# Optimization experiments

Measured on AMD Instinct MI355X. Metric: run time of the kernel, lower is better.

Reference implementation:

```python
import jax, jax.numpy as jnp
import numpy as np

DT = 0.01          # integration timestep
TH_HI = 1.0        # upper firing threshold
TH_LO = -1.0       # lower firing threshold


def setup_inputs() -> dict:
    key = jax.random.key(0)
    inputs = jax.random.normal(key, (64, 256, 1024), dtype=jnp.float32)
    return {"inputs": inputs}


def reference(inputs):
    # inputs: [B, T, D] pre-activation drive at each timestep
    rates = jnp.tanh(inputs)                     # activation(inputs), [B, T, D]
    x = jnp.swapaxes(rates, 0, 1)                # [T, B, D] for scan over time

    def step(v, r):
        v = v + r * DT                           # integrate
        sp = (v >= TH_HI).astype(v.dtype)        # positive spike
        sn = (v <= TH_LO).astype(v.dtype)        # negative spike
        v = v - sp * TH_HI - sn * TH_LO          # subtractive (self-regulating) reset
        out = (sp - sn) / DT                     # signed spike train scaled by 1/dt
        return v, out

    v0 = jnp.zeros(x.shape[1:], dtype=x.dtype)   # initial membrane state
    _, spikes = jax.lax.scan(step, v0, x)        # spikes: [T, B, D]
    spikes = jnp.swapaxes(spikes, 0, 1)          # [B, T, D]

    # spiking-aware (straight-through) output: spikes forward, rates gradient
    out = rates + jax.lax.stop_gradient(spikes - rates)
    return out
```

## Files before the change

kernel.cpp:

```cpp
#include <hip/hip_runtime.h>

#define B_DIM 64
#define T_STEPS 256
#define D_DIM 1024
#define CT 32
#define CHUNKS (T_STEPS / CT)
#define TPB 256

typedef __attribute__((address_space(3))) void lds_void;
typedef __attribute__((address_space(1))) const void glob_void;

__device__ __forceinline__ float xla_tanhf(float x) {
    const float kClamp = 7.90531110763549805f;
    float xc = fminf(fmaxf(x, -kClamp), kClamp);
    float x2 = xc * xc;
    float p = __builtin_fmaf(x2, -2.76076847742355e-16f, 2.00018790482477e-13f);
    p = __builtin_fmaf(x2, p, -8.60467152213735e-11f);
    p = __builtin_fmaf(x2, p, 5.12229709037114e-08f);
    p = __builtin_fmaf(x2, p, 1.48572235717979e-05f);
    p = __builtin_fmaf(x2, p, 6.37261928875436e-04f);
    p = __builtin_fmaf(x2, p, 4.89352455891786e-03f);
    p = xc * p;
    float q = __builtin_fmaf(x2, 1.19825839466702e-06f, 1.18534705686654e-04f);
    q = __builtin_fmaf(x2, q, 2.26843463243900e-03f);
    q = __builtin_fmaf(x2, q, 4.89352518554385e-03f);
    float r = p / q;
    return (fabsf(x) < 0.0004f) ? x : r;
}

__global__ __launch_bounds__(TPB, 1)
void spike_scan_kernel(const float* __restrict__ in, float* __restrict__ out) {
    __shared__ float buf[2][CT][TPB];

    const int tid = threadIdx.x;
    const int blk = blockIdx.x;
    const int b   = blk >> 2;
    const int d0  = (blk & 3) << 8;
    const size_t base = (size_t)b * (T_STEPS * D_DIM) + d0;
    const float* ip = in + base;
    float* op = out + base + tid;

    const int wave = tid >> 6;
    const int lane = tid & 63;

    auto stage = [&](int c, int pp) {
        const float* g0 = ip + (size_t)(c * CT + wave * 8) * D_DIM + lane * 4;
        #pragma unroll
        for (int r = 0; r < 8; ++r) {
            __builtin_amdgcn_global_load_lds(
                (glob_void*)(g0 + (size_t)r * D_DIM),
                (lds_void*)&buf[pp][wave * 8 + r][0],
                16, 0, 0);
        }
    };

    stage(0, 0);
    float v = 0.0f;

    for (int c = 0; c < CHUNKS; ++c) {
        const int pp = c & 1;
        __syncthreads();
        if (c + 1 < CHUNKS) stage(c + 1, pp ^ 1);

        float* opc = op + (size_t)c * CT * D_DIM;
        #pragma unroll
        for (int u = 0; u < CT; ++u) {
            float r = xla_tanhf(buf[pp][u][tid]);
            v = __builtin_fmaf(r, 0.01f, v);
            float sp = (v >= 1.0f)  ? 1.0f : 0.0f;
            float sn = (v <= -1.0f) ? 1.0f : 0.0f;
            v = (v - sp) + sn;
            __builtin_nontemporal_store((sp - sn) * 100.0f, opc + (size_t)u * D_DIM);
        }
    }
}

extern "C" void kernel_launch(void* const* d_in, const int* in_sizes, int n_in,
                              void* d_out, int out_size, void* d_ws, size_t ws_size,
                              hipStream_t stream) {
    const float* in = (const float*)d_in[0];
    float* out = (float*)d_out;
    dim3 block(TPB);
    dim3 grid(B_DIM * (D_DIM / TPB));
    spike_scan_kernel<<<grid, block, 0, stream>>>(in, out);
}
```

Measured before the change: 115.2 us.

## Replace LDS staging with register double-buffered inline-asm loads and stores

Drops the global_load_lds staging buffer and __syncthreads, so each thread loads its own column into two 16-element register buffers. Loads and nontemporal stores are issued with inline asm using 32-bit offsets, and explicit vmcnt waits order them. Store counts are folded into the waits. The chunk size shrinks to 16 and the launch-bounds occupancy hint is removed. The aim is to cut LDS round trips and barrier stalls in a latency-bound streaming scan, but the manual waitcnt accounting is fragile and the 32-bit offsets limit the tensor size.

```diff
diff --git a/kernel.cpp b/kernel.cpp
--- a/kernel.cpp
+++ b/kernel.cpp
@@ -1,14 +1,12 @@
 #include <hip/hip_runtime.h>
+#include <stdint.h>
 
 #define B_DIM 64
 #define T_STEPS 256
 #define D_DIM 1024
-#define CT 32
+#define CT 16
 #define CHUNKS (T_STEPS / CT)
 #define TPB 256
-
-typedef __attribute__((address_space(3))) void lds_void;
-typedef __attribute__((address_space(1))) const void glob_void;
 
 __device__ __forceinline__ float xla_tanhf(float x) {
     const float kClamp = 7.90531110763549805f;
@@ -28,51 +26,67 @@
     return (fabsf(x) < 0.0004f) ? x : r;
 }
 
-__global__ __launch_bounds__(TPB, 1)
+#define LD(i) "global_load_dword %" #i ", %16, %17\n\t" \
+              "v_add_u32 %16, 0x1000, %16\n\t"
+
+#define ISSUE16(B) asm volatile( \
+    LD(0) LD(1) LD(2) LD(3) LD(4) LD(5) LD(6) LD(7) \
+    LD(8) LD(9) LD(10) LD(11) LD(12) LD(13) LD(14) LD(15) \
+    : "=v"(B[0]), "=v"(B[1]), "=v"(B[2]), "=v"(B[3]), \
+      "=v"(B[4]), "=v"(B[5]), "=v"(B[6]), "=v"(B[7]), \
+      "=v"(B[8]), "=v"(B[9]), "=v"(B[10]), "=v"(B[11]), \
+      "=v"(B[12]), "=v"(B[13]), "=v"(B[14]), "=v"(B[15]), \
+      "+v"(voffi) \
+    : "s"(inp_u) : "memory")
+
+#define WAITBUF(B, CNT) asm volatile("s_waitcnt vmcnt(" CNT ")" \
+    : "+v"(B[0]), "+v"(B[1]), "+v"(B[2]), "+v"(B[3]), \
+      "+v"(B[4]), "+v"(B[5]), "+v"(B[6]), "+v"(B[7]), \
+      "+v"(B[8]), "+v"(B[9]), "+v"(B[10]), "+v"(B[11]), \
+      "+v"(B[12]), "+v"(B[13]), "+v"(B[14]), "+v"(B[15]) \
+    :: "memory")
+
+#define COMPUTE16(B) \
+    _Pragma("unroll") \
+    for (int u = 0; u < CT; ++u) { \
+        float r = xla_tanhf(B[u]); \
+        v = __builtin_fmaf(r, 0.01f, v); \
+        float sp = (v >= 1.0f)  ? 1.0f : 0.0f; \
+        float sn = (v <= -1.0f) ? 1.0f : 0.0f; \
+        v = (v - sp) + sn; \
+        float o = (sp - sn) * 100.0f; \
+        asm volatile("global_store_dword %0, %1, %2 nt\n\t" \
+                     "v_add_u32 %0, 0x1000, %0" \
+                     : "+v"(voffo) : "v"(o), "s"(outp_u) : "memory"); \
+    }
+
+#define CHUNK_MID(CUR, NXT) do { ISSUE16(NXT); WAITBUF(CUR, "32"); COMPUTE16(CUR); } while (0)
+
+__global__ __launch_bounds__(TPB)
 void spike_scan_kernel(const float* __restrict__ in, float* __restrict__ out) {
-    __shared__ float buf[2][CT][TPB];
+    const int gid = blockIdx.x * blockDim.x + threadIdx.x;
+    const int b = gid >> 10;
+    const int d = gid & (D_DIM - 1);
+    const uint32_t base_bytes = ((uint32_t)b * (T_STEPS * D_DIM) + (uint32_t)d) * 4u;
 
-    const int tid = threadIdx.x;
-    const int blk = blockIdx.x;
-    const int b   = blk >> 2;
-    const int d0  = (blk & 3) << 8;
-    const size_t base = (size_t)b * (T_STEPS * D_DIM) + d0;
-    const float* ip = in + base;
-    float* op = out + base + tid;
+    uint32_t voffi = base_bytes;
+    uint32_t voffo = base_bytes;
+    const uint64_t inp_u  = (uint64_t)in;
+    const uint64_t outp_u = (uint64_t)out;
 
-    const int wave = tid >> 6;
-    const int lane = tid & 63;
-
-    auto stage = [&](int c, int pp) {
-        const float* g0 = ip + (size_t)(c * CT + wave * 8) * D_DIM + lane * 4;
-        #pragma unroll
-        for (int r = 0; r < 8; ++r) {
-            __builtin_amdgcn_global_load_lds(
-                (glob_void*)(g0 + (size_t)r * D_DIM),
-                (lds_void*)&buf[pp][wave * 8 + r][0],
-                16, 0, 0);
-        }
-    };
-
-    stage(0, 0);
+    float bufA[CT], bufB[CT];
     float v = 0.0f;
 
-    for (int c = 0; c < CHUNKS; ++c) {
-        const int pp = c & 1;
-        __syncthreads();
-        if (c + 1 < CHUNKS) stage(c + 1, pp ^ 1);
-
-        float* opc = op + (size_t)c * CT * D_DIM;
-        #pragma unroll
-        for (int u = 0; u < CT; ++u) {
-            float r = xla_tanhf(buf[pp][u][tid]);
-            v = __builtin_fmaf(r, 0.01f, v);
-            float sp = (v >= 1.0f)  ? 1.0f : 0.0f;
-            float sn = (v <= -1.0f) ? 1.0f : 0.0f;
-            v = (v - sp) + sn;
-            __builtin_nontemporal_store((sp - sn) * 100.0f, opc + (size_t)u * D_DIM);
-        }
+    ISSUE16(bufA);
+    ISSUE16(bufB); WAITBUF(bufA, "16"); COMPUTE16(bufA);
+    CHUNK_MID(bufB, bufA);
+    #pragma unroll 1
+    for (int c2 = 1; c2 <= 6; ++c2) {
+        CHUNK_MID(bufA, bufB);
+        CHUNK_MID(bufB, bufA);
     }
+    CHUNK_MID(bufA, bufB);
+    WAITBUF(bufB, "16"); COMPUTE16(bufB);
 }
 
 extern "C" void kernel_launch(void* const* d_in, const int* in_sizes, int n_in,
@@ -81,6 +95,6 @@
     const float* in = (const float*)d_in[0];
     float* out = (float*)d_out;
     dim3 block(TPB);
-    dim3 grid(B_DIM * (D_DIM / TPB));
+    dim3 grid((B_DIM * D_DIM) / TPB);
     spike_scan_kernel<<<grid, block, 0, stream>>>(in, out);
 }
```

Result: faster. 112.2 us (-2.7%).

## Split block into producer waves for load+tanh and consumer waves for scan

Applied to the files above, without the earlier changes.

The kernel now uses 512-thread blocks with warp specialization. Four waves prefetch input into registers as float4, apply tanh, and write activations into a double-buffered LDS tile of 16 timesteps. The other four waves run the sequential spike integration from LDS and write outputs. This takes tanh off the serial recurrence and overlaps loading with the scan. In exchange, the async global-to-LDS loads and nontemporal stores are dropped, and the block pays one extra barrier per chunk with a smaller chunk size.

```diff
diff --git a/kernel.cpp b/kernel.cpp
--- a/kernel.cpp
+++ b/kernel.cpp
@@ -1,14 +1,13 @@
 #include <hip/hip_runtime.h>
+#include <stdint.h>
 
 #define B_DIM 64
 #define T_STEPS 256
 #define D_DIM 1024
-#define CT 32
+#define CT 16
 #define CHUNKS (T_STEPS / CT)
-#define TPB 256
-
-typedef __attribute__((address_space(3))) void lds_void;
-typedef __attribute__((address_space(1))) const void glob_void;
+#define TPB 512
+#define DSLICE 256
 
 __device__ __forceinline__ float xla_tanhf(float x) {
     const float kClamp = 7.90531110763549805f;
@@ -28,49 +27,68 @@
     return (fabsf(x) < 0.0004f) ? x : r;
 }
 
-__global__ __launch_bounds__(TPB, 1)
+__global__ __launch_bounds__(TPB)
 void spike_scan_kernel(const float* __restrict__ in, float* __restrict__ out) {
-    __shared__ float buf[2][CT][TPB];
+    __shared__ float lds_r[2][CT][DSLICE];
 
     const int tid = threadIdx.x;
     const int blk = blockIdx.x;
     const int b   = blk >> 2;
     const int d0  = (blk & 3) << 8;
     const size_t base = (size_t)b * (T_STEPS * D_DIM) + d0;
-    const float* ip = in + base;
-    float* op = out + base + tid;
+    const int wave = tid >> 6;
 
-    const int wave = tid >> 6;
-    const int lane = tid & 63;
+    if (wave < 4) {
+        const int lane = tid & 63;
+        const int w = wave;
+        const float* gp = in + base + (size_t)(4 * w) * D_DIM + 4 * lane;
 
-    auto stage = [&](int c, int pp) {
-        const float* g0 = ip + (size_t)(c * CT + wave * 8) * D_DIM + lane * 4;
+        float4 cur[4], nxt[4];
         #pragma unroll
-        for (int r = 0; r < 8; ++r) {
-            __builtin_amdgcn_global_load_lds(
-                (glob_void*)(g0 + (size_t)r * D_DIM),
-                (lds_void*)&buf[pp][wave * 8 + r][0],
-                16, 0, 0);
+        for (int r = 0; r < 4; ++r)
+            cur[r] = *(const float4*)(gp + (size_t)r * D_DIM);
+
+        #pragma unroll 1
+        for (int c = 0; c < CHUNKS; ++c) {
+            if (c + 1 < CHUNKS) {
+                const float* gn = gp + (size_t)(c + 1) * CT * D_DIM;
+                #pragma unroll
+                for (int r = 0; r < 4; ++r)
+                    nxt[r] = *(const float4*)(gn + (size_t)r * D_DIM);
+            }
+            const int pp = c & 1;
+            #pragma unroll
+            for (int r = 0; r < 4; ++r) {
+                float4 t4;
+                t4.x = xla_tanhf(cur[r].x);
+                t4.y = xla_tanhf(cur[r].y);
+                t4.z = xla_tanhf(cur[r].z);
+                t4.w = xla_tanhf(cur[r].w);
+                *(float4*)&lds_r[pp][4 * w + r][4 * lane] = t4;
+            }
+            __syncthreads();
+            #pragma unroll
+            for (int r = 0; r < 4; ++r) cur[r] = nxt[r];
         }
-    };
+    } else {
+        const int ctid = tid - 256;
+        float* op = out + base + ctid;
+        float v = 0.0f;
 
-    stage(0, 0);
-    float v = 0.0f;
-
-    for (int c = 0; c < CHUNKS; ++c) {
-        const int pp = c & 1;
-        __syncthreads();
-        if (c + 1 < CHUNKS) stage(c + 1, pp ^ 1);
-
-        float* opc = op + (size_t)c * CT * D_DIM;
-        #pragma unroll
-        for (int u = 0; u < CT; ++u) {
-            float r = xla_tanhf(buf[pp][u][tid]);
-            v = __builtin_fmaf(r, 0.01f, v);
-            float sp = (v >= 1.0f)  ? 1.0f : 0.0f;
-            float sn = (v <= -1.0f) ? 1.0f : 0.0f;
-            v = (v - sp) + sn;
-            __builtin_nontemporal_store((sp - sn) * 100.0f, opc + (size_t)u * D_DIM);
+        #pragma unroll 1
+        for (int c = 0; c < CHUNKS; ++c) {
+            __syncthreads();
+            const int pp = c & 1;
+            float* opc = op + (size_t)c * CT * D_DIM;
+            #pragma unroll
+            for (int u = 0; u < CT; ++u) {
+                float r = lds_r[pp][u][ctid];
+                v = __builtin_fmaf(r, 0.01f, v);
+                float sp = (v >= 1.0f)  ? 1.0f : 0.0f;
+                float sn = (v <= -1.0f) ? 1.0f : 0.0f;
+                v = (v - sp) + sn;
+                opc[(size_t)u * D_DIM] = (sp - sn) * 100.0f;
+            }
         }
     }
 }
@@ -81,6 +99,6 @@
     const float* in = (const float*)d_in[0];
     float* out = (float*)d_out;
     dim3 block(TPB);
-    dim3 grid(B_DIM * (D_DIM / TPB));
+    dim3 grid(B_DIM * (D_DIM / DSLICE));
     spike_scan_kernel<<<grid, block, 0, stream>>>(in, out);
 }
```

Result: slower. 119.5 us (+3.7%).

## Prefetch input chunks in registers and stage outputs through LDS for float4 stores

Applied to the files above, without the earlier changes.

Replaces the async global-to-LDS double buffer with a register-held float4 prefetch of the next chunk, written into a single LDS input tile each iteration. Outputs are gathered into an LDS tile and written back as coalesced float4 stores instead of per-thread scalar nontemporal stores. The launch bound no longer pins one block per CU, so more blocks may share a CU. In exchange it adds two barriers per chunk and more register pressure from the prefetch and the 32-element tanh array, and it drops the nontemporal hint on stores.

```diff
diff --git a/kernel.cpp b/kernel.cpp
--- a/kernel.cpp
+++ b/kernel.cpp
@@ -1,4 +1,5 @@
 #include <hip/hip_runtime.h>
+#include <stdint.h>
 
 #define B_DIM 64
 #define T_STEPS 256
@@ -6,9 +7,7 @@
 #define CT 32
 #define CHUNKS (T_STEPS / CT)
 #define TPB 256
-
-typedef __attribute__((address_space(3))) void lds_void;
-typedef __attribute__((address_space(1))) const void glob_void;
+#define DSLICE 256
 
 __device__ __forceinline__ float xla_tanhf(float x) {
     const float kClamp = 7.90531110763549805f;
@@ -28,49 +27,68 @@
     return (fabsf(x) < 0.0004f) ? x : r;
 }
 
-__global__ __launch_bounds__(TPB, 1)
+__device__ __forceinline__ void wg_barrier() {
+    asm volatile("s_waitcnt lgkmcnt(0)\n\ts_barrier" ::: "memory");
+}
+
+__global__ __launch_bounds__(TPB)
 void spike_scan_kernel(const float* __restrict__ in, float* __restrict__ out) {
-    __shared__ float buf[2][CT][TPB];
+    __shared__ float lds_in[CT][DSLICE];
+    __shared__ float lds_out[CT][DSLICE];
 
     const int tid = threadIdx.x;
     const int blk = blockIdx.x;
     const int b   = blk >> 2;
     const int d0  = (blk & 3) << 8;
     const size_t base = (size_t)b * (T_STEPS * D_DIM) + d0;
-    const float* ip = in + base;
-    float* op = out + base + tid;
+    const int w = tid >> 6;
+    const int l = tid & 63;
 
-    const int wave = tid >> 6;
-    const int lane = tid & 63;
+    const float* inb = in + base;
+    float* outb = out + base;
 
-    auto stage = [&](int c, int pp) {
-        const float* g0 = ip + (size_t)(c * CT + wave * 8) * D_DIM + lane * 4;
-        #pragma unroll
-        for (int r = 0; r < 8; ++r) {
-            __builtin_amdgcn_global_load_lds(
-                (glob_void*)(g0 + (size_t)r * D_DIM),
-                (lds_void*)&buf[pp][wave * 8 + r][0],
-                16, 0, 0);
-        }
-    };
+    float4 cur[8];
+    #pragma unroll
+    for (int r = 0; r < 8; ++r)
+        cur[r] = ((const float4*)(inb + (size_t)(8 * w + r) * D_DIM))[l];
 
-    stage(0, 0);
     float v = 0.0f;
 
+    #pragma unroll 1
     for (int c = 0; c < CHUNKS; ++c) {
-        const int pp = c & 1;
-        __syncthreads();
-        if (c + 1 < CHUNKS) stage(c + 1, pp ^ 1);
+        #pragma unroll
+        for (int r = 0; r < 8; ++r)
+            *(float4*)&lds_in[8 * w + r][4 * l] = cur[r];
+        wg_barrier();
 
-        float* opc = op + (size_t)c * CT * D_DIM;
+        if (c + 1 < CHUNKS) {
+            const float* inn = inb + (size_t)(c + 1) * CT * D_DIM;
+            #pragma unroll
+            for (int r = 0; r < 8; ++r)
+                cur[r] = ((const float4*)(inn + (size_t)(8 * w + r) * D_DIM))[l];
+        }
+        __builtin_amdgcn_sched_barrier(0);
+
+        float rr[CT];
+        #pragma unroll
+        for (int u = 0; u < CT; ++u) rr[u] = lds_in[u][tid];
+        #pragma unroll
+        for (int u = 0; u < CT; ++u) rr[u] = xla_tanhf(rr[u]);
         #pragma unroll
         for (int u = 0; u < CT; ++u) {
-            float r = xla_tanhf(buf[pp][u][tid]);
-            v = __builtin_fmaf(r, 0.01f, v);
+            v = __builtin_fmaf(rr[u], 0.01f, v);
             float sp = (v >= 1.0f)  ? 1.0f : 0.0f;
             float sn = (v <= -1.0f) ? 1.0f : 0.0f;
             v = (v - sp) + sn;
-            __builtin_nontemporal_store((sp - sn) * 100.0f, opc + (size_t)u * D_DIM);
+            lds_out[u][tid] = (sp - sn) * 100.0f;
+        }
+        wg_barrier();
+
+        float* outc = outb + (size_t)c * CT * D_DIM;
+        #pragma unroll
+        for (int r = 0; r < 8; ++r) {
+            float4 o4 = *(const float4*)&lds_out[8 * w + r][4 * l];
+            ((float4*)(outc + (size_t)(8 * w + r) * D_DIM))[l] = o4;
         }
     }
 }
@@ -81,6 +99,6 @@
     const float* in = (const float*)d_in[0];
     float* out = (float*)d_out;
     dim3 block(TPB);
-    dim3 grid(B_DIM * (D_DIM / TPB));
+    dim3 grid(B_DIM * (D_DIM / DSLICE));
     spike_scan_kernel<<<grid, block, 0, stream>>>(in, out);
 }
```

After: 139.1 us. 1.21x slower.
